# Kernel tuning notes

Measured on AMD Instinct MI355X. Metric: run time of the kernel, lower is better.

## Reference

```python
import jax, jax.numpy as jnp
import numpy as np

N = 65536        # batch (nodes)
IN_SIZE = 256    # irreps1.dim * irreps2.dim = 16*16
OUT_SIZE = 256
NNZ = 2048       # nonzero Clebsch-Gordan entries


def setup_inputs() -> dict:
    key = jax.random.key(0)
    k1, k2, k3, k4 = jax.random.split(key, 4)
    inp = jax.random.normal(k1, (N, IN_SIZE), dtype=jnp.float32)
    scale = jax.random.normal(k2, (NNZ,), dtype=jnp.float32)
    M_in = jax.random.randint(k3, (NNZ,), 0, IN_SIZE, dtype=jnp.int64)
    M = jnp.sort(jax.random.randint(k4, (NNZ,), 0, OUT_SIZE, dtype=jnp.int64))
    return {"input": inp, "scale": scale, "M_in": M_in, "M": M, "out_size": OUT_SIZE}


def reference(input, scale, M_in, M, out_size):
    # sparse_scale: out[n, M[k]] += scale[k] * input[n, M_in[k]]
    gathered = input[:, M_in] * scale  # [N, nnz]
    # segment-sum over the nnz axis into out_size output slots (M is sorted)
    out = jax.ops.segment_sum(gathered.T, M, num_segments=out_size,
                              indices_are_sorted=True).T  # [N, out_size]
    return out
```

## Files before the change

kernel.cpp:

```cpp
#include <hip/hip_runtime.h>
#include <hip/hip_bf16.h>

#define IN_SZ   256
#define OUT_SZ  256
#define NNZ_C   2048
#define NB      16
#define BM      128
#define BK      64

typedef __attribute__((ext_vector_type(8))) short bf16x8;
typedef __attribute__((ext_vector_type(4))) float f32x4;

static __device__ __forceinline__ short f2bf(float f) {
    __hip_bfloat16 h = __float2bfloat16(f);
    return (short)__builtin_bit_cast(unsigned short, h);
}


__global__ void build_w(const float* __restrict__ scale,
                        const int*   __restrict__ M_in,
                        const int*   __restrict__ M,
                        unsigned short* __restrict__ wb)
{
    __shared__ float row[IN_SZ];
    const int j = blockIdx.x;
    const int t = threadIdx.x;

#pragma unroll
    for (int i = t; i < IN_SZ; i += 64) row[i] = 0.f;

    int lo = 0, hi = NNZ_C;
    while (lo < hi) { int mid = (lo + hi) >> 1; if (M[mid] < j)     lo  = mid + 1; else hi  = mid; }
    int lo2 = lo, hi2 = NNZ_C;
    while (lo2 < hi2) { int mid = (lo2 + hi2) >> 1; if (M[mid] < j + 1) lo2 = mid + 1; else hi2 = mid; }

    __syncthreads();
    for (int k = lo + t; k < lo2; k += 64)
        atomicAdd(&row[M_in[k]], scale[k]);
    __syncthreads();

    const int wn = j >> 6, n = (j >> 4) & 3, l15 = j & 15;
#pragma unroll
    for (int kk = t; kk < IN_SZ; kk += 64) {
        int kt = kk >> 6, kf = (kk >> 5) & 1, lhi = (kk >> 3) & 3, e = kk & 7;
        int lane = lhi * 16 + l15;
        int c = (((wn * 4 + n) * 4 + kt) * 2 + kf) * 64 + lane;
        wb[c * 8 + e] = (unsigned short)f2bf(row[kk]);
    }
}


__global__ __launch_bounds__(512, 4)
void gemm_bm128(const float* __restrict__ input,
                const bf16x8* __restrict__ wfrag,
                float* __restrict__ out)
{
    __shared__ float sA[2][BM * BK];

    const int tid  = threadIdx.x;
    const int lane = tid & 63;
    const int wid  = tid >> 6;
    const int wm   = wid >> 2;
    const int wn   = wid & 3;
    const int l15  = lane & 15, lhi = lane >> 4;
    const long row0 = (long)blockIdx.x * BM;

    auto stage = [&](int buf, int kt) {
#pragma unroll
        for (int it = 0; it < 4; ++it) {
            const int c = wid * 4 + it;
            const int r = c * 4 + lhi;
            const int g = l15 ^ (r & 7);
            const float* src = input + (row0 + r) * IN_SZ + kt * BK + g * 4;
            __builtin_amdgcn_global_load_lds(
                (const __attribute__((address_space(1))) unsigned int*)src,
                (__attribute__((address_space(3))) unsigned int*)&sA[buf][c * 256],
                16, 0, 0);
        }
    };

    f32x4 acc[4][4];
#pragma unroll
    for (int m = 0; m < 4; ++m)
#pragma unroll
        for (int n = 0; n < 4; ++n)
            acc[m][n] = (f32x4){0.f, 0.f, 0.f, 0.f};

    bf16x8 Breg[2][8];

    stage(0, 0);
#pragma unroll
    for (int i = 0; i < 8; ++i)
        Breg[0][i] = wfrag[(((wn * 4 + (i >> 1)) * 4 + 0) * 2 + (i & 1)) * 64 + lane];
    __syncthreads();

#pragma unroll
    for (int kt = 0; kt < 4; ++kt) {
        const int cur = kt & 1;
        if (kt < 3) {
            stage(cur ^ 1, kt + 1);
#pragma unroll
            for (int i = 0; i < 8; ++i)
                Breg[cur ^ 1][i] =
                    wfrag[(((wn * 4 + (i >> 1)) * 4 + (kt + 1)) * 2 + (i & 1)) * 64 + lane];
        }

#pragma unroll
        for (int kf = 0; kf < 2; ++kf) {
#pragma unroll
            for (int m = 0; m < 4; ++m) {
                const int r  = wm * 64 + m * 16 + l15;
                const int g0 = kf * 8 + lhi * 2;
                f32x4 a0 = *(const f32x4*)&sA[cur][r * BK + (((g0    ) ^ (r & 7)) << 2)];
                f32x4 a1 = *(const f32x4*)&sA[cur][r * BK + (((g0 + 1) ^ (r & 7)) << 2)];
                bf16x8 u;
                u[0] = f2bf(a0[0]); u[1] = f2bf(a0[1]);
                u[2] = f2bf(a0[2]); u[3] = f2bf(a0[3]);
                u[4] = f2bf(a1[0]); u[5] = f2bf(a1[1]);
                u[6] = f2bf(a1[2]); u[7] = f2bf(a1[3]);
#pragma unroll
                for (int n = 0; n < 4; ++n)
                    acc[m][n] = __builtin_amdgcn_mfma_f32_16x16x32_bf16(
                        u, Breg[cur][n * 2 + kf], acc[m][n], 0, 0, 0);
            }
        }
        if (kt < 3) __syncthreads();
    }

#pragma unroll
    for (int m = 0; m < 4; ++m) {
        long r0 = row0 + wm * 64 + m * 16 + lhi * 4;
#pragma unroll
        for (int n = 0; n < 4; ++n) {
            int col = wn * 64 + n * 16 + l15;
#pragma unroll
            for (int r = 0; r < 4; ++r)
                out[(r0 + r) * OUT_SZ + col] = acc[m][n][r];
        }
    }
}


__global__ __launch_bounds__(256, 4)
void sparse_tp_kernel(const float* __restrict__ input,
                      const float* __restrict__ scale,
                      const int*   __restrict__ M_in,
                      const int*   __restrict__ M,
                      float*       __restrict__ out,
                      int N)
{
    __shared__ float s_in[NB * IN_SZ];
    __shared__ float s_scale[NNZ_C];
    __shared__ int   s_min[NNZ_C];
    __shared__ int   s_seg[OUT_SZ + 1];

    const int tid  = threadIdx.x;
    const int base = blockIdx.x * NB;

    {
        const float4* sc4  = reinterpret_cast<const float4*>(scale);
        const int4*   mi4  = reinterpret_cast<const int4*>(M_in);
        float4*       ssc4 = reinterpret_cast<float4*>(s_scale);
        int4*         smi4 = reinterpret_cast<int4*>(s_min);
        for (int v = tid; v < NNZ_C / 4; v += 256) { ssc4[v] = sc4[v]; smi4[v] = mi4[v]; }
    }
    {
        const float4* in4 = reinterpret_cast<const float4*>(input + (size_t)base * IN_SZ);
        float4*       si4 = reinterpret_cast<float4*>(s_in);
        for (int v = tid; v < NB * IN_SZ / 4; v += 256) {
            int row = v / (IN_SZ / 4);
            if (base + row < N) si4[v] = in4[v];
        }
    }
    {
        int j = tid, lo = 0, hi = NNZ_C;
        while (lo < hi) { int mid = (lo + hi) >> 1; if (M[mid] < j) lo = mid + 1; else hi = mid; }
        s_seg[j] = lo;
        if (tid == 0) s_seg[OUT_SZ] = NNZ_C;
    }
    __syncthreads();

    float acc[NB];
#pragma unroll
    for (int i = 0; i < NB; ++i) acc[i] = 0.f;

    const int j = tid;
    const int k1 = s_seg[j + 1];
    for (int k = s_seg[j]; k < k1; ++k) {
        const float s = s_scale[k];
        const int   m = s_min[k];
#pragma unroll
        for (int i = 0; i < NB; ++i) acc[i] += s * s_in[i * IN_SZ + m];
    }

    float* orow = out + (size_t)base * OUT_SZ + j;
#pragma unroll
    for (int i = 0; i < NB; ++i)
        if (base + i < N) orow[(size_t)i * OUT_SZ] = acc[i];
}


extern "C" void kernel_launch(void* const* d_in, const int* in_sizes, int n_in,
                              void* d_out, int out_size, void* d_ws, size_t ws_size,
                              hipStream_t stream)
{
    const float* input = (const float*)d_in[0];
    const float* scale = (const float*)d_in[1];
    const int*   M_in  = (const int*)d_in[2];
    const int*   M     = (const int*)d_in[3];
    float*       out   = (float*)d_out;

    const int N = in_sizes[0] / IN_SZ;

    if (ws_size >= (size_t)(128 * 1024) && (N % BM) == 0) {
        unsigned short* wb = (unsigned short*)d_ws;
        build_w   <<<OUT_SZ, 64, 0, stream>>>(scale, M_in, M, wb);
        gemm_bm128<<<N / BM, 512, 0, stream>>>(input, (const bf16x8*)wb, out);
    } else {
        sparse_tp_kernel<<<(N + NB - 1) / NB, 256, 0, stream>>>(input, scale, M_in, M, out, N);
    }
}
```

Baseline: 131.0 us.

## Triple-buffer A tiles with explicit vmcnt waits in smaller-block GEMM

Replaces the 128-row, 512-thread double-buffered GEMM with a 64-row, 256-thread kernel that triple-buffers the A tile in LDS. The K loop is unrolled by hand, and partial s_waitcnt vmcnt counts plus raw s_barrier keep two stages of global-to-LDS loads in flight while MFMA runs. This aims to hide HBM latency better and to raise block count and occupancy on this memory-bound op. In exchange it relies on hand-counted vmcnt values being correct, and each block now reloads the full B fragment for only half as many rows.

```diff
diff --git a/kernel.cpp b/kernel.cpp
--- a/kernel.cpp
+++ b/kernel.cpp
@@ -5,7 +5,7 @@
 #define OUT_SZ  256
 #define NNZ_C   2048
 #define NB      16
-#define BM      128
+#define BM      64
 #define BK      64
 
 typedef __attribute__((ext_vector_type(8))) short bf16x8;
@@ -50,25 +50,23 @@
 }
 
 
-__global__ __launch_bounds__(512, 4)
-void gemm_bm128(const float* __restrict__ input,
-                const bf16x8* __restrict__ wfrag,
-                float* __restrict__ out)
-{
-    __shared__ float sA[2][BM * BK];
+__global__ __launch_bounds__(256, 3)
+void gemm_pipe(const float* __restrict__ input,
+               const bf16x8* __restrict__ wfrag,
+               float* __restrict__ out)
+{
+    __shared__ float sA[3][BM * BK];
 
     const int tid  = threadIdx.x;
     const int lane = tid & 63;
-    const int wid  = tid >> 6;
-    const int wm   = wid >> 2;
-    const int wn   = wid & 3;
+    const int w    = tid >> 6;
     const int l15  = lane & 15, lhi = lane >> 4;
     const long row0 = (long)blockIdx.x * BM;
 
     auto stage = [&](int buf, int kt) {
 #pragma unroll
         for (int it = 0; it < 4; ++it) {
-            const int c = wid * 4 + it;
+            const int c = w * 4 + it;
             const int r = c * 4 + lhi;
             const int g = l15 ^ (r & 7);
             const float* src = input + (row0 + r) * IN_SZ + kt * BK + g * 4;
@@ -78,6 +76,11 @@
                 16, 0, 0);
         }
     };
+    auto loadB = [&](bf16x8* dst, int kt) {
+#pragma unroll
+        for (int i = 0; i < 8; ++i)
+            dst[i] = wfrag[(((w * 4 + (i >> 1)) * 4 + kt) * 2 + (i & 1)) * 64 + lane];
+    };
 
     f32x4 acc[4][4];
 #pragma unroll
@@ -86,33 +89,15 @@
         for (int n = 0; n < 4; ++n)
             acc[m][n] = (f32x4){0.f, 0.f, 0.f, 0.f};
 
-    bf16x8 Breg[2][8];
-
-    stage(0, 0);
-#pragma unroll
-    for (int i = 0; i < 8; ++i)
-        Breg[0][i] = wfrag[(((wn * 4 + (i >> 1)) * 4 + 0) * 2 + (i & 1)) * 64 + lane];
-    __syncthreads();
-
-#pragma unroll
-    for (int kt = 0; kt < 4; ++kt) {
-        const int cur = kt & 1;
-        if (kt < 3) {
-            stage(cur ^ 1, kt + 1);
-#pragma unroll
-            for (int i = 0; i < 8; ++i)
-                Breg[cur ^ 1][i] =
-                    wfrag[(((wn * 4 + (i >> 1)) * 4 + (kt + 1)) * 2 + (i & 1)) * 64 + lane];
-        }
-
-#pragma unroll
-        for (int kf = 0; kf < 2; ++kf) {
+    auto compute = [&](int buf, const bf16x8* B) {
+#pragma unroll
+        for (int kf = 0; kf < 2; ++kf)
 #pragma unroll
             for (int m = 0; m < 4; ++m) {
-                const int r  = wm * 64 + m * 16 + l15;
+                const int r  = m * 16 + l15;
                 const int g0 = kf * 8 + lhi * 2;
-                f32x4 a0 = *(const f32x4*)&sA[cur][r * BK + (((g0    ) ^ (r & 7)) << 2)];
-                f32x4 a1 = *(const f32x4*)&sA[cur][r * BK + (((g0 + 1) ^ (r & 7)) << 2)];
+                f32x4 a0 = *(const f32x4*)&sA[buf][r * BK + (((g0    ) ^ (r & 7)) << 2)];
+                f32x4 a1 = *(const f32x4*)&sA[buf][r * BK + (((g0 + 1) ^ (r & 7)) << 2)];
                 bf16x8 u;
                 u[0] = f2bf(a0[0]); u[1] = f2bf(a0[1]);
                 u[2] = f2bf(a0[2]); u[3] = f2bf(a0[3]);
@@ -121,18 +106,47 @@
 #pragma unroll
                 for (int n = 0; n < 4; ++n)
                     acc[m][n] = __builtin_amdgcn_mfma_f32_16x16x32_bf16(
-                        u, Breg[cur][n * 2 + kf], acc[m][n], 0, 0, 0);
+                        u, B[n * 2 + kf], acc[m][n], 0, 0, 0);
             }
-        }
-        if (kt < 3) __syncthreads();
-    }
+    };
+
+    bf16x8 Breg[2][8];
+
+    stage(0, 0);
+    loadB(Breg[0], 0);
+    stage(1, 1);
+
+    asm volatile("s_waitcnt vmcnt(12)" ::: "memory");
+    __builtin_amdgcn_s_barrier();
+    __builtin_amdgcn_sched_barrier(0);
+    loadB(Breg[1], 1);
+    compute(0, Breg[0]);
+    stage(2, 2);
+
+    asm volatile("s_waitcnt vmcnt(12)" ::: "memory");
+    __builtin_amdgcn_s_barrier();
+    __builtin_amdgcn_sched_barrier(0);
+    loadB(Breg[0], 2);
+    compute(1, Breg[1]);
+    stage(0, 3);
+
+    asm volatile("s_waitcnt vmcnt(12)" ::: "memory");
+    __builtin_amdgcn_s_barrier();
+    __builtin_amdgcn_sched_barrier(0);
+    loadB(Breg[1], 3);
+    compute(2, Breg[0]);
+
+    asm volatile("s_waitcnt vmcnt(8)" ::: "memory");
+    __builtin_amdgcn_s_barrier();
+    __builtin_amdgcn_sched_barrier(0);
+    compute(0, Breg[1]);
 
 #pragma unroll
     for (int m = 0; m < 4; ++m) {
-        long r0 = row0 + wm * 64 + m * 16 + lhi * 4;
+        long r0 = row0 + m * 16 + lhi * 4;
 #pragma unroll
         for (int n = 0; n < 4; ++n) {
-            int col = wn * 64 + n * 16 + l15;
+            int col = w * 64 + n * 16 + l15;
 #pragma unroll
             for (int r = 0; r < 4; ++r)
                 out[(r0 + r) * OUT_SZ + col] = acc[m][n][r];
@@ -214,8 +228,8 @@
 
     if (ws_size >= (size_t)(128 * 1024) && (N % BM) == 0) {
         unsigned short* wb = (unsigned short*)d_ws;
-        build_w   <<<OUT_SZ, 64, 0, stream>>>(scale, M_in, M, wb);
-        gemm_bm128<<<N / BM, 512, 0, stream>>>(input, (const bf16x8*)wb, out);
+        build_w  <<<OUT_SZ, 64, 0, stream>>>(scale, M_in, M, wb);
+        gemm_pipe<<<N / BM, 256, 0, stream>>>(input, (const bf16x8*)wb, out);
     } else {
         sparse_tp_kernel<<<(N + NB - 1) / NB, 256, 0, stream>>>(input, scale, M_in, M, out, N);
     }
```

Result: no change. 132.2 us (+1.0%).
